# Optimization experiments

Hardware: AMD Instinct MI355X
Metric: run time of the kernel (lower is better)

## Reference

```python
import jax, jax.numpy as jnp
import numpy as np

B = 128          # batch
D = 2048         # original_dim
P = 16000        # projection_dim


def _count_sketch_matrix(key, d, p):
    """Dense count-sketch matrix: one +/-1 per row at a random column.
    Mirrors the torch init: col ~ randint(0, p-1), sign = 2*randint(0,2)-1."""
    k_idx, k_sgn = jax.random.split(key)
    idx = jax.random.randint(k_idx, (d,), 0, p - 1)            # torch uses high=p-1 (exclusive)
    sgn = (2 * jax.random.randint(k_sgn, (d,), 0, 2) - 1).astype(jnp.float32)
    C = jnp.zeros((d, p), dtype=jnp.float32)
    return C.at[jnp.arange(d), idx].set(sgn)


def setup_inputs() -> dict:
    key = jax.random.key(0)
    kx1, kx2, kc1, kc2 = jax.random.split(key, 4)
    x1 = jax.random.normal(kx1, (B, D), dtype=jnp.float32)
    x2 = jax.random.normal(kx2, (B, D), dtype=jnp.float32)
    C1 = _count_sketch_matrix(kc1, D, P)
    C2 = _count_sketch_matrix(kc2, D, P)
    return {"x1": x1, "x2": x2, "C1": C1, "C2": C2}


def reference(x1, x2, C1, C2):
    # Count-sketch projections (dense mm, as in the original module)
    y1 = x1 @ C1                      # [B, P]
    y2 = x2 @ C2                      # [B, P]
    # Circular convolution via FFT -> elementwise complex multiply -> IFFT.
    # Original takes only the real part of the IFFT output.
    f1 = jnp.fft.fft(y1, axis=-1)
    f2 = jnp.fft.fft(y2, axis=-1)
    phi = jnp.fft.ifft(f1 * f2, axis=-1).real.astype(jnp.float32)
    return phi                        # [B, P]
```

## Files before the change

kernel.cpp:

```cpp
#include <hip/hip_runtime.h>

#define NFFT 16000
#define BATCH 128
#define DIM 2048
#define TP 17

__device__ __forceinline__ float2 cmul(float2 a, float2 b) {
    return make_float2(a.x * b.x - a.y * b.y, a.x * b.y + a.y * b.x);
}
__device__ __forceinline__ float2 cadd(float2 a, float2 b) { return make_float2(a.x + b.x, a.y + b.y); }
__device__ __forceinline__ float2 csub(float2 a, float2 b) { return make_float2(a.x - b.x, a.y - b.y); }
__device__ __forceinline__ float2 cis(float ang) { return make_float2(__cosf(ang), __sinf(ang)); }

__device__ __forceinline__ int rev5_3(int n) {
    int d0 = n % 5, r = n / 5;
    int d1 = r % 5, d2 = r / 5;
    return d0 * 25 + d1 * 5 + d2;
}

__device__ __forceinline__ float2 conjG(float2 Zk, float2 Zm) {
    float u = (Zk.x * Zk.x - Zk.y * Zk.y) - (Zm.x * Zm.x - Zm.y * Zm.y);
    float v = 2.f * (Zk.x * Zk.y + Zm.x * Zm.y);
    return make_float2(0.25f * v, 0.25f * u);
}

__device__ __forceinline__ void dif128(float2& x0, float2& x1, int l) {
    const float PI_F = 3.14159265358979323846f;
    {
        float2 a = x0, b = x1;
        x0 = cadd(a, b);
        float2 d = csub(a, b);
        x1 = cmul(d, cis(-PI_F / 64.0f * (float)l));
    }
    #pragma unroll
    for (int m = 32; m >= 1; m >>= 1) {
        int j = l & (m - 1);
        bool upper = (l & m) != 0;
        float2 w = cis(-PI_F / (float)m * (float)j);
        float2 o0, o1;
        o0.x = __shfl_xor(x0.x, m); o0.y = __shfl_xor(x0.y, m);
        o1.x = __shfl_xor(x1.x, m); o1.y = __shfl_xor(x1.y, m);
        if (upper) {
            x0 = cmul(csub(o0, x0), w);
            x1 = cmul(csub(o1, x1), w);
        } else {
            x0 = cadd(x0, o0);
            x1 = cadd(x1, o1);
        }
    }
}

__global__ void extract_sketch(const float* __restrict__ C1, const float* __restrict__ C2,
                               int* __restrict__ idx1, float* __restrict__ sgn1,
                               int* __restrict__ idx2, float* __restrict__ sgn2) {
    int gwave = (blockIdx.x * blockDim.x + threadIdx.x) >> 6;
    int lane = threadIdx.x & 63;
    if (gwave >= 2 * DIM) return;
    const float* row;
    int* idxp; float* sgnp; int d;
    if (gwave < DIM) { d = gwave;       row = C1 + (size_t)d * NFFT; idxp = idx1; sgnp = sgn1; }
    else             { d = gwave - DIM; row = C2 + (size_t)d * NFFT; idxp = idx2; sgnp = sgn2; }
    for (int step = 0; step < 16; ++step) {
        int off0 = step * 1024 + lane * 4;
        float4 v[4];
        #pragma unroll
        for (int c = 0; c < 4; ++c) {
            int off = off0 + c * 256;
            v[c] = (off < NFFT) ? *reinterpret_cast<const float4*>(row + off)
                                : make_float4(0.f, 0.f, 0.f, 0.f);
        }
        bool found = false;
        #pragma unroll
        for (int c = 0; c < 4; ++c) {
            float4 w = v[c];
            if (w.x != 0.f || w.y != 0.f || w.z != 0.f || w.w != 0.f) {
                int off = off0 + c * 256;
                int j; float s;
                if (w.x != 0.f)      { j = 0; s = w.x; }
                else if (w.y != 0.f) { j = 1; s = w.y; }
                else if (w.z != 0.f) { j = 2; s = w.z; }
                else                 { j = 3; s = w.w; }
                idxp[d] = off + j;
                sgnp[d] = s;
                found = true;
            }
        }
        if (__any(found)) return;
    }
}

__global__ void __launch_bounds__(256) k1_colfft(
        const float* __restrict__ x1, const float* __restrict__ x2,
        const int* __restrict__ idx1, const float* __restrict__ sgn1,
        const int* __restrict__ idx2, const float* __restrict__ sgn2,
        float2* __restrict__ U) {
    __shared__ float2 S[32 * 125];
    const int b = blockIdx.x >> 2, q = blockIdx.x & 3;
    const int tid = threadIdx.x;

    for (int i = tid; i < 32 * 125; i += 256) S[i] = make_float2(0.f, 0.f);
    __syncthreads();

    const float* x1b = x1 + (size_t)b * DIM;
    const float* x2b = x2 + (size_t)b * DIM;
    for (int d = tid; d < DIM; d += 256) {
        int p1 = idx1[d]; int n1a = p1 & 127;
        if ((n1a >> 5) == q) atomicAdd(&S[(n1a & 31) * 125 + rev5_3(p1 >> 7)].x, sgn1[d] * x1b[d]);
        int p2 = idx2[d]; int n1b = p2 & 127;
        if ((n1b >> 5) == q) atomicAdd(&S[(n1b & 31) * 125 + rev5_3(p2 >> 7)].y, sgn2[d] * x2b[d]);
    }
    __syncthreads();

    const float C1_5 = 0.30901699437494742f, S1_5 = 0.95105651629515357f;
    const float C2_5 = -0.80901699437494745f, S2_5 = 0.58778525229247312f;
    const float2 w5tab[5] = { make_float2(1.f, 0.f),
                              make_float2(C1_5, -S1_5), make_float2(C2_5, -S2_5),
                              make_float2(C2_5,  S2_5), make_float2(C1_5,  S1_5) };
    #pragma unroll
    for (int s = 0; s < 3; ++s) {
        const int m = (s == 0) ? 1 : (s == 1) ? 5 : 25;
        const float angstep = -6.28318530717958647692f / (float)(5 * m);
        for (int task = tid; task < 32 * 25; task += 256) {
            int row = task / 25;
            int bf = task - row * 25;
            int t = bf % m, blk = bf / m;
            int base = row * 125 + blk * (5 * m) + t;
            float2 xv[5];
            #pragma unroll
            for (int r = 0; r < 5; ++r) xv[r] = S[base + r * m];
            if (m > 1) {
                float2 w1 = cis(angstep * (float)t);
                float2 w2 = cmul(w1, w1), w3 = cmul(w2, w1), w4 = cmul(w2, w2);
                xv[1] = cmul(xv[1], w1); xv[2] = cmul(xv[2], w2);
                xv[3] = cmul(xv[3], w3); xv[4] = cmul(xv[4], w4);
            }
            float2 y[5];
            #pragma unroll
            for (int qq = 0; qq < 5; ++qq) {
                float2 acc = xv[0];
                #pragma unroll
                for (int r = 1; r < 5; ++r) {
                    float2 t2 = cmul(xv[r], w5tab[(qq * r) % 5]);
                    acc.x += t2.x; acc.y += t2.y;
                }
                y[qq] = acc;
            }
            #pragma unroll
            for (int qq = 0; qq < 5; ++qq) S[base + qq * m] = y[qq];
        }
        __syncthreads();
    }

    const float ANGN = -6.28318530717958647692f / 16000.0f;
    const int n1base = q * 32;
    float2* Ub = U + (size_t)b * NFFT;
    for (int i = tid; i < 32 * 125; i += 256) {
        int n1l = i & 31, k2 = i >> 5;
        int n1 = n1base + n1l;
        Ub[k2 * 128 + n1] = cmul(S[n1l * 125 + k2], cis(ANGN * (float)(n1 * k2)));
    }
}

__global__ void __launch_bounds__(256) k2_pair(const float2* __restrict__ U,
                                               float2* __restrict__ V) {
    __shared__ float2 Z[4][2][128];
    const int w = threadIdx.x >> 6, l = threadIdx.x & 63;
    const int task = blockIdx.x * 4 + w;
    const int b = task / 63, cg = task - b * 63;
    const int c = cg, cm = (cg == 0) ? 0 : 125 - cg;
    const float2* Ub = U + (size_t)b * NFFT;

    float2 a0 = Ub[c * 128 + l],  a1 = Ub[c * 128 + l + 64];
    float2 b0 = Ub[cm * 128 + l], b1 = Ub[cm * 128 + l + 64];
    dif128(a0, a1, l);
    dif128(b0, b1, l);
    const int e = (int)(__brev((unsigned)l) >> 25);

    Z[w][0][e] = a0; Z[w][0][e + 1] = a1;
    Z[w][1][e] = b0; Z[w][1][e + 1] = b1;
    __syncthreads();

    float2 gA0, gA1, gB0, gB1;
    if (cg != 0) {
        float2 zm0 = Z[w][1][127 - e];
        float2 zm1 = Z[w][1][126 - e];
        gA0 = conjG(a0, zm0);
        gA1 = conjG(a1, zm1);
        gB1 = conjG(zm0, a0);
        gB0 = conjG(zm1, a1);
    } else {
        float2 zm0 = Z[w][0][(128 - e) & 127];
        float2 zm1 = Z[w][0][127 - e];
        gA0 = conjG(a0, zm0);
        gA1 = conjG(a1, zm1);
        gB0 = make_float2(0.f, 0.f); gB1 = make_float2(0.f, 0.f);
    }
    __syncthreads();

    Z[w][0][e] = gA0; Z[w][0][e + 1] = gA1;
    if (cg != 0) { Z[w][1][126 - e] = gB0; Z[w][1][127 - e] = gB1; }
    __syncthreads();

    float2 p0 = Z[w][0][l], p1 = Z[w][0][l + 64];
    float2 q0 = Z[w][1][l], q1 = Z[w][1][l + 64];
    dif128(p0, p1, l);
    dif128(q0, q1, l);

    const float ANGN = -6.28318530717958647692f / 16000.0f;
    float2* Vb = V + (size_t)b * NFFT;
    p0 = cmul(p0, cis(ANGN * (float)(c * e)));
    p1 = cmul(p1, cis(ANGN * (float)(c * (e + 1))));
    *reinterpret_cast<float4*>(&Vb[c * 128 + e]) = make_float4(p0.x, p0.y, p1.x, p1.y);
    if (cg != 0) {
        q0 = cmul(q0, cis(ANGN * (float)(cm * e)));
        q1 = cmul(q1, cis(ANGN * (float)(cm * (e + 1))));
        *reinterpret_cast<float4*>(&Vb[cm * 128 + e]) = make_float4(q0.x, q0.y, q1.x, q1.y);
    }
}

__global__ void __launch_bounds__(256) k3_rowfft(const float2* __restrict__ V,
                                                 float* __restrict__ out) {
    __shared__ float2 T[125 * TP];
    const int b = blockIdx.x >> 3, g = blockIdx.x & 7;
    const int j1base = g * 16, tid = threadIdx.x;
    const float2* Vb = V + (size_t)b * NFFT;

    for (int i = tid; i < 125 * 16; i += 256) {
        int m1 = i >> 4, j1l = i & 15;
        T[rev5_3(m1) * TP + j1l] = Vb[m1 * 128 + j1base + j1l];
    }
    __syncthreads();

    const float C1_5 = 0.30901699437494742f, S1_5 = 0.95105651629515357f;
    const float C2_5 = -0.80901699437494745f, S2_5 = 0.58778525229247312f;
    const float2 w5tab[5] = { make_float2(1.f, 0.f),
                              make_float2(C1_5, -S1_5), make_float2(C2_5, -S2_5),
                              make_float2(C2_5,  S2_5), make_float2(C1_5,  S1_5) };
    #pragma unroll
    for (int s = 0; s < 3; ++s) {
        const int m = (s == 0) ? 1 : (s == 1) ? 5 : 25;
        const float angstep = -6.28318530717958647692f / (float)(5 * m);
        for (int task = tid; task < 16 * 25; task += 256) {
            int bf = task >> 4;
            int j1l = task & 15;
            int t = bf % m, blk = bf / m;
            int base = (blk * (5 * m) + t) * TP + j1l;
            float2 xv[5];
            #pragma unroll
            for (int r = 0; r < 5; ++r) xv[r] = T[base + r * m * TP];
            if (m > 1) {
                float2 w1 = cis(angstep * (float)t);
                float2 w2 = cmul(w1, w1), w3 = cmul(w2, w1), w4 = cmul(w2, w2);
                xv[1] = cmul(xv[1], w1); xv[2] = cmul(xv[2], w2);
                xv[3] = cmul(xv[3], w3); xv[4] = cmul(xv[4], w4);
            }
            float2 y[5];
            #pragma unroll
            for (int qq = 0; qq < 5; ++qq) {
                float2 acc = xv[0];
                #pragma unroll
                for (int r = 1; r < 5; ++r) {
                    float2 t2 = cmul(xv[r], w5tab[(qq * r) % 5]);
                    acc.x += t2.x; acc.y += t2.y;
                }
                y[qq] = acc;
            }
            #pragma unroll
            for (int qq = 0; qq < 5; ++qq) T[base + qq * m * TP] = y[qq];
        }
        __syncthreads();
    }

    const float invN = 1.0f / (float)NFFT;
    float* outb = out + (size_t)b * NFFT;
    for (int i = tid; i < 125 * 16; i += 256) {
        int j2 = i >> 4, j1l = i & 15;
        outb[j1base + j1l + 128 * j2] = T[j2 * TP + j1l].x * invN;
    }
}

extern "C" void kernel_launch(void* const* d_in, const int* in_sizes, int n_in,
                              void* d_out, int out_size, void* d_ws, size_t ws_size,
                              hipStream_t stream) {
    (void)in_sizes; (void)n_in; (void)out_size; (void)ws_size;
    const float* x1 = (const float*)d_in[0];
    const float* x2 = (const float*)d_in[1];
    const float* C1 = (const float*)d_in[2];
    const float* C2 = (const float*)d_in[3];
    float* out = (float*)d_out;

    char* w = (char*)d_ws;
    int*    idx1 = (int*)  (w);
    float*  sgn1 = (float*)(w + 8192);
    int*    idx2 = (int*)  (w + 16384);
    float*  sgn2 = (float*)(w + 24576);
    float2* U    = (float2*)(w + 32768);
    float2* V    = (float2*)(w + 32768 + 16384000);

    extract_sketch<<<(2 * DIM) / 4, 256, 0, stream>>>(C1, C2, idx1, sgn1, idx2, sgn2);
    k1_colfft     <<<BATCH * 4, 256, 0, stream>>>(x1, x2, idx1, sgn1, idx2, sgn2, U);
    k2_pair       <<<2016, 256, 0, stream>>>(U, V);
    k3_rowfft     <<<BATCH * 8, 256, 0, stream>>>(V, out);
}
```

Baseline: 302.0 us.

## Replace k2 shared-memory exchanges with wave shuffles and precompute FFT twiddles

The pair kernel drops its shared-memory scratch and the three block barriers, and instead swaps conjugate-symmetric partners and the bit-reversal permutation within each wave using shuffles. Per-lane twiddles for the 128-point DIF FFT are computed once and reused across all four FFT calls rather than recomputed each time. The second column's FFT is skipped when cg is zero. The column-FFT kernel also moves from 256 to 512 threads per block, which adds parallelism but may lower occupancy or raise atomic contention.

```diff
diff --git a/kernel.cpp b/kernel.cpp
--- a/kernel.cpp
+++ b/kernel.cpp
@@ -17,6 +17,14 @@
     int d1 = r % 5, d2 = r / 5;
     return d0 * 25 + d1 * 5 + d2;
 }
+__device__ __forceinline__ int rev7(int x) { return (int)(__brev((unsigned)x) >> 25); }
+
+__device__ __forceinline__ float2 shfl2(float2 v, int lane) {
+    return make_float2(__shfl(v.x, lane), __shfl(v.y, lane));
+}
+__device__ __forceinline__ float2 shfl2_xor(float2 v, int mask) {
+    return make_float2(__shfl_xor(v.x, mask), __shfl_xor(v.y, mask));
+}
 
 __device__ __forceinline__ float2 conjG(float2 Zk, float2 Zm) {
     float u = (Zk.x * Zk.x - Zk.y * Zk.y) - (Zm.x * Zm.x - Zm.y * Zm.y);
@@ -24,23 +32,18 @@
     return make_float2(0.25f * v, 0.25f * u);
 }
 
-__device__ __forceinline__ void dif128(float2& x0, float2& x1, int l) {
-    const float PI_F = 3.14159265358979323846f;
+__device__ __forceinline__ void dif128(float2& x0, float2& x1, const float2* tw, int l) {
     {
         float2 a = x0, b = x1;
         x0 = cadd(a, b);
-        float2 d = csub(a, b);
-        x1 = cmul(d, cis(-PI_F / 64.0f * (float)l));
-    }
+        x1 = cmul(csub(a, b), tw[0]);
+    }
+    int s = 1;
     #pragma unroll
-    for (int m = 32; m >= 1; m >>= 1) {
-        int j = l & (m - 1);
-        bool upper = (l & m) != 0;
-        float2 w = cis(-PI_F / (float)m * (float)j);
-        float2 o0, o1;
-        o0.x = __shfl_xor(x0.x, m); o0.y = __shfl_xor(x0.y, m);
-        o1.x = __shfl_xor(x1.x, m); o1.y = __shfl_xor(x1.y, m);
-        if (upper) {
+    for (int m = 32; m >= 1; m >>= 1, ++s) {
+        float2 w = tw[s];
+        float2 o0 = shfl2_xor(x0, m), o1 = shfl2_xor(x1, m);
+        if (l & m) {
             x0 = cmul(csub(o0, x0), w);
             x1 = cmul(csub(o1, x1), w);
         } else {
@@ -89,7 +92,7 @@
     }
 }
 
-__global__ void __launch_bounds__(256) k1_colfft(
+__global__ void __launch_bounds__(512) k1_colfft(
         const float* __restrict__ x1, const float* __restrict__ x2,
         const int* __restrict__ idx1, const float* __restrict__ sgn1,
         const int* __restrict__ idx2, const float* __restrict__ sgn2,
@@ -98,12 +101,12 @@
     const int b = blockIdx.x >> 2, q = blockIdx.x & 3;
     const int tid = threadIdx.x;
 
-    for (int i = tid; i < 32 * 125; i += 256) S[i] = make_float2(0.f, 0.f);
+    for (int i = tid; i < 32 * 125; i += 512) S[i] = make_float2(0.f, 0.f);
     __syncthreads();
 
     const float* x1b = x1 + (size_t)b * DIM;
     const float* x2b = x2 + (size_t)b * DIM;
-    for (int d = tid; d < DIM; d += 256) {
+    for (int d = tid; d < DIM; d += 512) {
         int p1 = idx1[d]; int n1a = p1 & 127;
         if ((n1a >> 5) == q) atomicAdd(&S[(n1a & 31) * 125 + rev5_3(p1 >> 7)].x, sgn1[d] * x1b[d]);
         int p2 = idx2[d]; int n1b = p2 & 127;
@@ -120,7 +123,7 @@
     for (int s = 0; s < 3; ++s) {
         const int m = (s == 0) ? 1 : (s == 1) ? 5 : 25;
         const float angstep = -6.28318530717958647692f / (float)(5 * m);
-        for (int task = tid; task < 32 * 25; task += 256) {
+        for (int task = tid; task < 32 * 25; task += 512) {
             int row = task / 25;
             int bf = task - row * 25;
             int t = bf % m, blk = bf / m;
@@ -154,7 +157,7 @@
     const float ANGN = -6.28318530717958647692f / 16000.0f;
     const int n1base = q * 32;
     float2* Ub = U + (size_t)b * NFFT;
-    for (int i = tid; i < 32 * 125; i += 256) {
+    for (int i = tid; i < 32 * 125; i += 512) {
         int n1l = i & 31, k2 = i >> 5;
         int n1 = n1base + n1l;
         Ub[k2 * 128 + n1] = cmul(S[n1l * 125 + k2], cis(ANGN * (float)(n1 * k2)));
@@ -163,58 +166,75 @@
 
 __global__ void __launch_bounds__(256) k2_pair(const float2* __restrict__ U,
                                                float2* __restrict__ V) {
-    __shared__ float2 Z[4][2][128];
     const int w = threadIdx.x >> 6, l = threadIdx.x & 63;
     const int task = blockIdx.x * 4 + w;
     const int b = task / 63, cg = task - b * 63;
-    const int c = cg, cm = (cg == 0) ? 0 : 125 - cg;
+    const int c = cg, cm = cg ? 125 - cg : 0;
     const float2* Ub = U + (size_t)b * NFFT;
-
-    float2 a0 = Ub[c * 128 + l],  a1 = Ub[c * 128 + l + 64];
-    float2 b0 = Ub[cm * 128 + l], b1 = Ub[cm * 128 + l + 64];
-    dif128(a0, a1, l);
-    dif128(b0, b1, l);
-    const int e = (int)(__brev((unsigned)l) >> 25);
-
-    Z[w][0][e] = a0; Z[w][0][e + 1] = a1;
-    Z[w][1][e] = b0; Z[w][1][e + 1] = b1;
-    __syncthreads();
+    const float PI_F = 3.14159265358979323846f;
+
+    float2 tw[7];
+    tw[0] = cis(-PI_F / 64.0f * (float)l);
+    {
+        int m = 32;
+        #pragma unroll
+        for (int s = 1; s < 7; ++s, m >>= 1)
+            tw[s] = cis(-PI_F / (float)m * (float)(l & (m - 1)));
+    }
+
+    float2 a0 = Ub[c * 128 + l], a1 = Ub[c * 128 + l + 64];
+    dif128(a0, a1, tw, l);
+    float2 b0, b1;
+    if (cg) {
+        b0 = Ub[cm * 128 + l]; b1 = Ub[cm * 128 + l + 64];
+        dif128(b0, b1, tw, l);
+    }
+
+    const int e  = rev7(l);
+    const int lp = rev7(126 - e);
 
     float2 gA0, gA1, gB0, gB1;
-    if (cg != 0) {
-        float2 zm0 = Z[w][1][127 - e];
-        float2 zm1 = Z[w][1][126 - e];
+    if (cg) {
+        float2 zm0 = shfl2(b1, lp);
+        float2 zm1 = shfl2(b0, lp);
         gA0 = conjG(a0, zm0);
         gA1 = conjG(a1, zm1);
-        gB1 = conjG(zm0, a0);
-        gB0 = conjG(zm1, a1);
+        float2 ym0 = shfl2(a1, lp);
+        float2 ym1 = shfl2(a0, lp);
+        gB0 = conjG(b0, ym0);
+        gB1 = conjG(b1, ym1);
     } else {
-        float2 zm0 = Z[w][0][(128 - e) & 127];
-        float2 zm1 = Z[w][0][127 - e];
+        int hz = rev7((128 - e) & 127);
+        float2 zm0 = shfl2(a0, hz);
+        float2 zm1 = shfl2(a1, lp);
         gA0 = conjG(a0, zm0);
         gA1 = conjG(a1, zm1);
-        gB0 = make_float2(0.f, 0.f); gB1 = make_float2(0.f, 0.f);
-    }
-    __syncthreads();
-
-    Z[w][0][e] = gA0; Z[w][0][e + 1] = gA1;
-    if (cg != 0) { Z[w][1][126 - e] = gB0; Z[w][1][127 - e] = gB1; }
-    __syncthreads();
-
-    float2 p0 = Z[w][0][l], p1 = Z[w][0][l + 64];
-    float2 q0 = Z[w][1][l], q1 = Z[w][1][l + 64];
-    dif128(p0, p1, l);
-    dif128(q0, q1, l);
-
+        gB0 = gB1 = make_float2(0.f, 0.f);
+    }
+
+    const int q = rev7(l & 62);
     const float ANGN = -6.28318530717958647692f / 16000.0f;
     float2* Vb = V + (size_t)b * NFFT;
-    p0 = cmul(p0, cis(ANGN * (float)(c * e)));
-    p1 = cmul(p1, cis(ANGN * (float)(c * (e + 1))));
-    *reinterpret_cast<float4*>(&Vb[c * 128 + e]) = make_float4(p0.x, p0.y, p1.x, p1.y);
-    if (cg != 0) {
-        q0 = cmul(q0, cis(ANGN * (float)(cm * e)));
-        q1 = cmul(q1, cis(ANGN * (float)(cm * (e + 1))));
-        *reinterpret_cast<float4*>(&Vb[cm * 128 + e]) = make_float4(q0.x, q0.y, q1.x, q1.y);
+
+    {
+        float2 t00 = shfl2(gA0, q),     t10 = shfl2(gA1, q);
+        float2 t01 = shfl2(gA0, q + 1), t11 = shfl2(gA1, q + 1);
+        float2 p0 = (l & 1) ? t10 : t00;
+        float2 p1 = (l & 1) ? t11 : t01;
+        dif128(p0, p1, tw, l);
+        p0 = cmul(p0, cis(ANGN * (float)(c * e)));
+        p1 = cmul(p1, cis(ANGN * (float)(c * (e + 1))));
+        *reinterpret_cast<float4*>(&Vb[c * 128 + e]) = make_float4(p0.x, p0.y, p1.x, p1.y);
+    }
+    if (cg) {
+        float2 t00 = shfl2(gB0, q),     t10 = shfl2(gB1, q);
+        float2 t01 = shfl2(gB0, q + 1), t11 = shfl2(gB1, q + 1);
+        float2 p0 = (l & 1) ? t10 : t00;
+        float2 p1 = (l & 1) ? t11 : t01;
+        dif128(p0, p1, tw, l);
+        p0 = cmul(p0, cis(ANGN * (float)(cm * e)));
+        p1 = cmul(p1, cis(ANGN * (float)(cm * (e + 1))));
+        *reinterpret_cast<float4*>(&Vb[cm * 128 + e]) = make_float4(p0.x, p0.y, p1.x, p1.y);
     }
 }
 
@@ -298,7 +318,7 @@
     float2* V    = (float2*)(w + 32768 + 16384000);
 
     extract_sketch<<<(2 * DIM) / 4, 256, 0, stream>>>(C1, C2, idx1, sgn1, idx2, sgn2);
-    k1_colfft     <<<BATCH * 4, 256, 0, stream>>>(x1, x2, idx1, sgn1, idx2, sgn2, U);
+    k1_colfft     <<<BATCH * 4, 512, 0, stream>>>(x1, x2, idx1, sgn1, idx2, sgn2, U);
     k2_pair       <<<2016, 256, 0, stream>>>(U, V);
     k3_rowfft     <<<BATCH * 8, 256, 0, stream>>>(V, out);
 }
```

Result: faster. 293.4 us (-2.9%).
